# Kernel optimization log

Hardware: AMD Instinct MI355X
Metric: run time of the kernel (lower is better)

Reference implementation:

```python
import jax, jax.numpy as jnp
import numpy as np

DIM = 1024
HEADS = 16
HEAD_DIM = DIM // HEADS
EPS = 1e-5


def _layer_norm(z, g, b):
    m = jnp.mean(z, axis=-1, keepdims=True)
    v = jnp.var(z, axis=-1, keepdims=True)
    return (z - m) * jax.lax.rsqrt(v + EPS) * g + b


def setup_inputs() -> dict:
    key = jax.random.key(0)
    ks = jax.random.split(key, 8)
    B, T, S = 2, 2048, 2048
    x = jax.random.normal(ks[0], (B, T, DIM), dtype=jnp.float32)
    context = jax.random.normal(ks[1], (B, S, DIM), dtype=jnp.float32)
    w_qkv = jax.random.normal(ks[2], (DIM, 3 * DIM), dtype=jnp.float32) * 0.02
    b_qkv = jnp.zeros((3 * DIM,), dtype=jnp.float32)
    w_out = jax.random.normal(ks[3], (DIM, DIM), dtype=jnp.float32) * 0.02
    b_out = jnp.zeros((DIM,), dtype=jnp.float32)
    ln_g = jnp.ones((DIM,), dtype=jnp.float32)
    ln_b = jnp.zeros((DIM,), dtype=jnp.float32)
    return {"x": x, "context": context, "w_qkv": w_qkv, "b_qkv": b_qkv,
            "w_out": w_out, "b_out": b_out, "ln_g": ln_g, "ln_b": ln_b}


def reference(x, context, w_qkv, b_qkv, w_out, b_out, ln_g, ln_b):
    B, T, C = x.shape
    S = context.shape[1]
    scale = HEAD_DIM ** -0.5

    def split_heads(z):  # [B, L, C] -> [B, H, L, Dh]
        return z.reshape(z.shape[0], z.shape[1], HEADS, HEAD_DIM).transpose(0, 2, 1, 3)

    # self qkv
    qkv = _layer_norm(x, ln_g, ln_b) @ w_qkv + b_qkv  # [B, T, 3C]
    q = split_heads(qkv[..., :C])
    k = split_heads(qkv[..., C:2 * C])
    v = split_heads(qkv[..., 2 * C:])

    # context k, v from the shared qkv projection (K/V slices)
    ckv = _layer_norm(context, ln_g, ln_b) @ w_qkv + b_qkv  # [B, S, 3C]
    ck = split_heads(ckv[..., C:2 * C])
    cv = split_heads(ckv[..., 2 * C:])

    k = jnp.concatenate([k, ck], axis=2)  # [B, H, T+S, Dh]
    v = jnp.concatenate([v, cv], axis=2)

    attn = jax.nn.softmax(jnp.einsum('bhtd,bhsd->bhts', q, k) * scale, axis=-1)
    out = jnp.einsum('bhts,bhsd->bhtd', attn, v)  # [B, H, T, Dh]
    out = out.transpose(0, 2, 1, 3).reshape(B, T, C)
    return out @ w_out + b_out + x
```

## Files before the change

kernel.cpp:

```cpp
#include <hip/hip_runtime.h>
#include <stdint.h>

#define H 16
#define DH 64
#define T 2048
#define SS 2048
#define L 4096
#define DIM 1024
#define BB 2

typedef __bf16 bf16x8 __attribute__((ext_vector_type(8)));
typedef float f32x4 __attribute__((ext_vector_type(4)));
typedef float f32x16 __attribute__((ext_vector_type(16)));
typedef unsigned u32x4 __attribute__((ext_vector_type(4)));

__device__ __forceinline__ unsigned short f2bf(float f){
  unsigned u = __builtin_bit_cast(unsigned, f);
  u += 0x7fff + ((u >> 16) & 1);
  return (unsigned short)(u >> 16);
}

__device__ __forceinline__ unsigned cvt_pk_bf16(float lo, float hi){
  unsigned r;
  asm("v_cvt_pk_bf16_f32 %0, %1, %2" : "=v"(r) : "v"(lo), "v"(hi));
  return r;
}

__device__ __forceinline__ float fmax3(float a, float b, float c){
  float r;
  asm("v_max3_f32 %0, %1, %2, %3" : "=v"(r) : "v"(a), "v"(b), "v"(c));
  return r;
}

__device__ __forceinline__ void gload_lds16(const void* g, void* l){
  void* gnc = const_cast<void*>(g);
  __builtin_amdgcn_global_load_lds((__attribute__((address_space(1))) void*)gnc,
                                   (__attribute__((address_space(3))) void*)l, 16, 0, 0);
}

__global__ __launch_bounds__(256) void ln_kernel(const float* __restrict__ x, const float* __restrict__ ctx,
                          const float* __restrict__ g, const float* __restrict__ b,
                          unsigned short* __restrict__ out){
  int row = blockIdx.x;
  int tid = threadIdx.x;
  const float* src = (row < BB*T) ? (x + (size_t)row*DIM) : (ctx + (size_t)(row - BB*T)*DIM);
  float4 v = reinterpret_cast<const float4*>(src)[tid];
  float s  = v.x + v.y + v.z + v.w;
  float s2 = v.x*v.x + v.y*v.y + v.z*v.z + v.w*v.w;
  #pragma unroll
  for (int off = 32; off > 0; off >>= 1){
    s  += __shfl_down(s,  off, 64);
    s2 += __shfl_down(s2, off, 64);
  }
  __shared__ float red[8];
  if ((tid & 63) == 0){ red[(tid>>6)*2] = s; red[(tid>>6)*2+1] = s2; }
  __syncthreads();
  s  = red[0] + red[2] + red[4] + red[6];
  s2 = red[1] + red[3] + red[5] + red[7];
  float mean = s * (1.0f/DIM);
  float var  = s2 * (1.0f/DIM) - mean*mean;
  float rstd = rsqrtf(var + 1e-5f);
  float4 gg = reinterpret_cast<const float4*>(g)[tid];
  float4 bv = reinterpret_cast<const float4*>(b)[tid];
  ushort4 o;
  o.x = f2bf((v.x-mean)*rstd*gg.x + bv.x);
  o.y = f2bf((v.y-mean)*rstd*gg.y + bv.y);
  o.z = f2bf((v.z-mean)*rstd*gg.z + bv.z);
  o.w = f2bf((v.w-mean)*rstd*gg.w + bv.w);
  reinterpret_cast<ushort4*>(out + (size_t)row*DIM)[tid] = o;
}

__global__ __launch_bounds__(256) void transpose_f32_bf16(const float* __restrict__ in,
                          unsigned short* __restrict__ out, int R, int C){
  __shared__ float tile[32][33];
  int c0 = blockIdx.x*32, r0 = blockIdx.y*32;
  int tx = threadIdx.x, ty = threadIdx.y;
  #pragma unroll
  for (int k = 0; k < 4; k++)
    tile[ty + k*8][tx] = in[(size_t)(r0 + ty + k*8)*C + c0 + tx];
  __syncthreads();
  #pragma unroll
  for (int k = 0; k < 4; k++)
    out[(size_t)(c0 + ty + k*8)*R + r0 + tx] = f2bf(tile[tx][ty + k*8]);
}

__global__ __launch_bounds__(256) void qkv_gemm(const unsigned short* __restrict__ A,
      const unsigned short* __restrict__ Bt, const float* __restrict__ bias,
      unsigned short* __restrict__ qbuf, unsigned short* __restrict__ kbuf,
      unsigned short* __restrict__ vtbuf){
  int orig = blockIdx.x;
  int wid = (orig & 7)*192 + (orig >> 3);
  int n0 = (wid % 24)*128, m0 = (wid / 24)*128;
  if (m0 >= BB*T && n0 < DIM) return;
  __shared__ union {
    struct { unsigned short at[128*32]; unsigned short bt[128*32]; } s;
    unsigned short ct[128][136];
    unsigned short vt[128][136];
  } u;
  int tid = threadIdx.x, lane = tid & 63, wv = tid >> 6;
  int wm = (wv >> 1)*64, wn = (wv & 1)*64;
  f32x4 acc[4][4];
  #pragma unroll
  for (int i = 0; i < 4; i++)
    #pragma unroll
    for (int j = 0; j < 4; j++) acc[i][j] = (f32x4){0.f,0.f,0.f,0.f};

  for (int k0 = 0; k0 < DIM; k0 += 32){
    #pragma unroll
    for (int c = 0; c < 2; c++){
      int idx = c*256 + tid;
      int row = idx >> 2, koff = (idx & 3)*16;
      gload_lds16((const char*)A  + ((size_t)(m0+row)*DIM + k0)*2 + koff,
                  (char*)u.s.at + (c*256 + wv*64)*16);
      gload_lds16((const char*)Bt + ((size_t)(n0+row)*DIM + k0)*2 + koff,
                  (char*)u.s.bt + (c*256 + wv*64)*16);
    }
    __syncthreads();
    bf16x8 af[4], bfv[4];
    #pragma unroll
    for (int i = 0; i < 4; i++){
      af[i]  = *reinterpret_cast<const bf16x8*>((const char*)u.s.at + (wm + i*16 + (lane&15))*64 + (lane>>4)*16);
      bfv[i] = *reinterpret_cast<const bf16x8*>((const char*)u.s.bt + (wn + i*16 + (lane&15))*64 + (lane>>4)*16);
    }
    #pragma unroll
    for (int mi = 0; mi < 4; mi++)
      #pragma unroll
      for (int ni = 0; ni < 4; ni++)
        acc[mi][ni] = __builtin_amdgcn_mfma_f32_16x16x32_bf16(af[mi], bfv[ni], acc[mi][ni], 0,0,0);
    __syncthreads();
  }

  int sec = n0 >> 10;
  if (sec < 2){
    float scale = (sec == 0) ? 0.18033688f : 1.0f;
    #pragma unroll
    for (int ni = 0; ni < 4; ni++){
      int nl = wn + ni*16 + (lane & 15);
      float bv = bias[n0 + nl];
      #pragma unroll
      for (int mi = 0; mi < 4; mi++){
        int ml = wm + mi*16 + ((lane >> 4) << 2);
        #pragma unroll
        for (int r = 0; r < 4; r++)
          u.ct[ml + r][nl] = f2bf((acc[mi][ni][r] + bv)*scale);
      }
    }
    __syncthreads();
    #pragma unroll
    for (int c = 0; c < 8; c++){
      int idx = c*256 + tid;
      int row = idx >> 4, ch = idx & 15;
      bf16x8 v = *reinterpret_cast<const bf16x8*>(&u.ct[row][ch*8]);
      int gm = m0 + row, gn = n0 + ch*8;
      int cc = gn & 1023, hh2 = cc >> 6, d = cc & 63;
      bool isctx = gm >= BB*T;
      int rm = isctx ? gm - BB*T : gm;
      int bidx = rm >> 11, tt = rm & 2047;
      size_t bh2 = (size_t)bidx*H + hh2;
      if (sec == 0){
        *reinterpret_cast<bf16x8*>(qbuf + (bh2*T + tt)*DH + d) = v;
      } else {
        int j = isctx ? T + tt : tt;
        *reinterpret_cast<bf16x8*>(kbuf + (bh2*L + j)*DH + d) = v;
      }
    }
  } else {
    #pragma unroll
    for (int ni = 0; ni < 4; ni++){
      int nl = wn + ni*16 + (lane & 15);
      float bv = bias[n0 + nl];
      #pragma unroll
      for (int mi = 0; mi < 4; mi++){
        int ml = wm + mi*16 + ((lane >> 4) << 2);
        ushort4 o;
        o.x = f2bf(acc[mi][ni][0] + bv);
        o.y = f2bf(acc[mi][ni][1] + bv);
        o.z = f2bf(acc[mi][ni][2] + bv);
        o.w = f2bf(acc[mi][ni][3] + bv);
        *reinterpret_cast<ushort4*>(&u.vt[nl][ml]) = o;
      }
    }
    __syncthreads();
    #pragma unroll
    for (int c = 0; c < 8; c++){
      int idx = c*256 + tid;
      int nl = idx >> 4, ch = idx & 15;
      bf16x8 v = *reinterpret_cast<const bf16x8*>(&u.vt[nl][ch*8]);
      int gn = n0 + nl;
      int cc = gn & 1023, hh2 = cc >> 6, d = cc & 63;
      int gm = m0 + ch*8;
      bool isctx = gm >= BB*T;
      int rm = isctx ? gm - BB*T : gm;
      int bidx = rm >> 11, tt = rm & 2047;
      int j = isctx ? T + tt : tt;
      size_t bh2 = (size_t)bidx*H + hh2;
      *reinterpret_cast<bf16x8*>(vtbuf + (bh2*DH + d)*L + j) = v;
    }
  }
}

__global__ __launch_bounds__(256, 4) void attn_kernel(const unsigned short* __restrict__ q,
      const unsigned short* __restrict__ kbuf, const unsigned short* __restrict__ vtbuf,
      unsigned short* __restrict__ obuf, float* __restrict__ mbuf, float* __restrict__ lbuf){
  int hw = blockIdx.x;
  int wid = (hw & 7)*128 + (hw >> 3);
  int qt = wid & 15, bh = (wid >> 4) & 31, cb = wid >> 9;
  int hh = bh & 15, b = bh >> 4;
  int tid = threadIdx.x, lane = tid & 63, wv = tid >> 6;
  int hi = lane >> 5, q32 = lane & 31;
  __shared__ unsigned short kt[2][64*64];
  __shared__ unsigned short vtt[2][64*64];
  size_t bhs = (size_t)b*H + hh;
  int qbase = qt*128 + wv*32;

  const unsigned short* qp = q + (bhs*T + qbase + q32)*DH + hi*8;
  bf16x8 qf[4];
  #pragma unroll
  for (int ks = 0; ks < 4; ks++)
    qf[ks] = *reinterpret_cast<const bf16x8*>(qp + ks*16);

  bf16x8 ones;
  #pragma unroll
  for (int j = 0; j < 8; j++) ones[j] = (__bf16)1.0f;

  f32x16 o_acc[2], l_vec;
  #pragma unroll
  for (int d = 0; d < 2; d++)
    #pragma unroll
    for (int i = 0; i < 16; i++) o_acc[d][i] = 0.f;
  #pragma unroll
  for (int i = 0; i < 16; i++) l_vec[i] = 0.f;
  float m_l = -1e30f;

  const char* kg = (const char*)(kbuf + bhs*(size_t)L*DH) + (size_t)cb*2048*128;
  const char* vg = (const char*)(vtbuf + bhs*(size_t)DH*L) + (size_t)cb*4096;

  #define STAGE(bufi, jt) { \
    _Pragma("unroll") \
    for (int c = 0; c < 2; c++){ \
      int idx = c*256 + tid; \
      int row = idx >> 3, c16 = idx & 7; \
      int sc16 = c16 ^ (row & 7); \
      gload_lds16(kg + (size_t)((jt)*64 + row)*128 + sc16*16, \
                  (char*)kt[bufi] + (c*256 + wv*64)*16); \
      gload_lds16(vg + (size_t)row*(L*2) + (jt)*128 + sc16*16, \
                  (char*)vtt[bufi] + (c*256 + wv*64)*16); \
    } }

  STAGE(0, 0);
  __syncthreads();

  for (int jt = 0; jt < 32; ++jt){
    int bufi = jt & 1;
    if (jt + 1 < 32) STAGE(bufi^1, jt+1);
    const char* kb = (const char*)kt[bufi];
    const char* vb = (const char*)vtt[bufi];

    f32x16 sc[2];
    #pragma unroll
    for (int t = 0; t < 2; t++)
      #pragma unroll
      for (int i = 0; i < 16; i++) sc[t][i] = 0.f;
    #pragma unroll
    for (int ks = 0; ks < 4; ks++){
      #pragma unroll
      for (int t = 0; t < 2; t++){
        int row = t*32 + q32;
        bf16x8 kf = *reinterpret_cast<const bf16x8*>(kb + row*128 + (((ks*2+hi) ^ (row&7))*16));
        sc[t] = __builtin_amdgcn_mfma_f32_32x32x16_bf16(kf, qf[ks], sc[t], 0,0,0);
      }
    }

    float rt[2];
    #pragma unroll
    for (int t = 0; t < 2; t++){
      float v0 = fmax3(sc[t][0],  sc[t][1],  sc[t][2]);
      float v1 = fmax3(sc[t][3],  sc[t][4],  sc[t][5]);
      float v2 = fmax3(sc[t][6],  sc[t][7],  sc[t][8]);
      float v3 = fmax3(sc[t][9],  sc[t][10], sc[t][11]);
      float v4 = fmax3(sc[t][12], sc[t][13], sc[t][14]);
      rt[t] = fmaxf(fmax3(v0, v1, v2), fmax3(v3, v4, sc[t][15]));
    }
    float tm = fmaxf(rt[0], rt[1]);

    if (!__all(tm - m_l <= 8.0f)){
      float tmf = fmaxf(tm, __shfl_xor(tm, 32, 64));
      float mn = fmaxf(m_l, tmf);
      float alpha = __builtin_amdgcn_exp2f(m_l - mn);
      m_l = mn;
      #pragma unroll
      for (int d = 0; d < 2; d++)
        #pragma unroll
        for (int i = 0; i < 16; i++) o_acc[d][i] *= alpha;
      l_vec[0] *= alpha;
    }
    #pragma unroll
    for (int t = 0; t < 2; t++)
      #pragma unroll
      for (int i = 0; i < 16; i++)
        sc[t][i] = __builtin_amdgcn_exp2f(sc[t][i] - m_l);

    bf16x8 pfrag[4];
    #pragma unroll
    for (int t = 0; t < 2; t++){
      #pragma unroll
      for (int half = 0; half < 2; half++){
        unsigned p01 = cvt_pk_bf16(sc[t][half*8+0], sc[t][half*8+1]);
        unsigned p23 = cvt_pk_bf16(sc[t][half*8+2], sc[t][half*8+3]);
        unsigned p45 = cvt_pk_bf16(sc[t][half*8+4], sc[t][half*8+5]);
        unsigned p67 = cvt_pk_bf16(sc[t][half*8+6], sc[t][half*8+7]);
        asm("v_permlane32_swap_b32 %0, %1" : "+v"(p01), "+v"(p45));
        asm("v_permlane32_swap_b32 %0, %1" : "+v"(p23), "+v"(p67));
        u32x4 w = (u32x4){p01, p23, p45, p67};
        pfrag[t*2 + half] = __builtin_bit_cast(bf16x8, w);
      }
    }

    #pragma unroll
    for (int ks = 0; ks < 4; ks++){
      #pragma unroll
      for (int d = 0; d < 2; d++){
        int row = d*32 + q32;
        bf16x8 vf = *reinterpret_cast<const bf16x8*>(vb + row*128 + (((ks*2+hi) ^ (row&7))*16));
        o_acc[d] = __builtin_amdgcn_mfma_f32_32x32x16_bf16(vf, pfrag[ks], o_acc[d], 0,0,0);
      }
      l_vec = __builtin_amdgcn_mfma_f32_32x32x16_bf16(ones, pfrag[ks], l_vec, 0,0,0);
    }
    __syncthreads();
  }

  float inv = 1.0f / l_vec[0];
  unsigned short* aop = obuf + (size_t)cb*BB*H*T*DH + ((size_t)bh*T + qbase + q32)*DH;
  #pragma unroll
  for (int d = 0; d < 2; d++)
    #pragma unroll
    for (int rg = 0; rg < 4; rg++){
      int d0 = d*32 + rg*8 + hi*4;
      ushort4 o;
      o.x = __builtin_bit_cast(unsigned short, (__bf16)(o_acc[d][rg*4+0]*inv));
      o.y = __builtin_bit_cast(unsigned short, (__bf16)(o_acc[d][rg*4+1]*inv));
      o.z = __builtin_bit_cast(unsigned short, (__bf16)(o_acc[d][rg*4+2]*inv));
      o.w = __builtin_bit_cast(unsigned short, (__bf16)(o_acc[d][rg*4+3]*inv));
      *reinterpret_cast<ushort4*>(aop + d0) = o;
    }
  if (hi == 0){
    size_t mi = ((size_t)cb*BB*H + bh)*T + qbase + q32;
    mbuf[mi] = m_l;
    lbuf[mi] = l_vec[0];
  }
}

__global__ __launch_bounds__(256) void attn_combine(const unsigned short* __restrict__ obuf,
      const float* __restrict__ mbuf, const float* __restrict__ lbuf,
      unsigned short* __restrict__ ao){
  int gid = blockIdx.x*256 + threadIdx.x;
  int d8 = gid & 7;
  int qg = gid >> 3;
  int qq = qg & (T-1);
  int bh = qg >> 11;
  int b = bh >> 4, h = bh & 15;
  float m0 = mbuf[(size_t)qg];
  float m1 = mbuf[(size_t)BB*H*T + qg];
  float l0 = lbuf[(size_t)qg];
  float l1 = lbuf[(size_t)BB*H*T + qg];
  float mm = fmaxf(m0, m1);
  float w0 = l0 * __builtin_amdgcn_exp2f(m0 - mm);
  float w1 = l1 * __builtin_amdgcn_exp2f(m1 - mm);
  float inv = 1.0f / (w0 + w1);
  w0 *= inv; w1 *= inv;
  bf16x8 o0 = *reinterpret_cast<const bf16x8*>(obuf + (size_t)qg*DH + d8*8);
  bf16x8 o1 = *reinterpret_cast<const bf16x8*>(obuf + (size_t)BB*H*T*DH + (size_t)qg*DH + d8*8);
  bf16x8 res;
  #pragma unroll
  for (int j = 0; j < 8; j++)
    res[j] = (__bf16)(w0*(float)o0[j] + w1*(float)o1[j]);
  *reinterpret_cast<bf16x8*>(ao + ((size_t)b*T + qq)*DIM + h*DH + d8*8) = res;
}

__global__ __launch_bounds__(256) void out_gemm(const unsigned short* __restrict__ A,
      const unsigned short* __restrict__ Bt, const float* __restrict__ bout,
      const float* __restrict__ xres, float* __restrict__ out){
  int n0 = blockIdx.x*128, m0 = blockIdx.y*128;
  __shared__ unsigned short at[128*32];
  __shared__ unsigned short btile[128*32];
  int tid = threadIdx.x, lane = tid & 63, wv = tid >> 6;
  int wm = (wv >> 1)*64, wn = (wv & 1)*64;
  f32x4 acc[4][4];
  #pragma unroll
  for (int i = 0; i < 4; i++)
    #pragma unroll
    for (int j = 0; j < 4; j++) acc[i][j] = (f32x4){0.f,0.f,0.f,0.f};

  for (int k0 = 0; k0 < DIM; k0 += 32){
    #pragma unroll
    for (int c = 0; c < 2; c++){
      int idx = c*256 + tid;
      int row = idx >> 2, koff = (idx & 3)*16;
      gload_lds16((const char*)A  + ((size_t)(m0+row)*DIM + k0)*2 + koff,
                  (char*)at + (c*256 + wv*64)*16);
      gload_lds16((const char*)Bt + ((size_t)(n0+row)*DIM + k0)*2 + koff,
                  (char*)btile + (c*256 + wv*64)*16);
    }
    __syncthreads();
    bf16x8 af[4], bfv[4];
    #pragma unroll
    for (int i = 0; i < 4; i++){
      af[i]  = *reinterpret_cast<const bf16x8*>((const char*)at    + (wm + i*16 + (lane&15))*64 + (lane>>4)*16);
      bfv[i] = *reinterpret_cast<const bf16x8*>((const char*)btile + (wn + i*16 + (lane&15))*64 + (lane>>4)*16);
    }
    #pragma unroll
    for (int mi = 0; mi < 4; mi++)
      #pragma unroll
      for (int ni = 0; ni < 4; ni++)
        acc[mi][ni] = __builtin_amdgcn_mfma_f32_16x16x32_bf16(af[mi], bfv[ni], acc[mi][ni], 0,0,0);
    __syncthreads();
  }

  #pragma unroll
  for (int ni = 0; ni < 4; ni++){
    int gn = n0 + wn + ni*16 + (lane & 15);
    float bv = bout[gn];
    #pragma unroll
    for (int mi = 0; mi < 4; mi++){
      int gmb = m0 + wm + mi*16 + ((lane >> 4) << 2);
      #pragma unroll
      for (int r = 0; r < 4; r++){
        int gm = gmb + r;
        out[(size_t)gm*DIM + gn] = acc[mi][ni][r] + bv + xres[(size_t)gm*DIM + gn];
      }
    }
  }
}

extern "C" void kernel_launch(void* const* d_in, const int* in_sizes, int n_in,
                              void* d_out, int out_size, void* d_ws, size_t ws_size,
                              hipStream_t stream){
  const float* x    = (const float*)d_in[0];
  const float* ctx  = (const float*)d_in[1];
  const float* wqkv = (const float*)d_in[2];
  const float* bqkv = (const float*)d_in[3];
  const float* wout = (const float*)d_in[4];
  const float* bout = (const float*)d_in[5];
  const float* lng  = (const float*)d_in[6];
  const float* lnb  = (const float*)d_in[7];
  float* out = (float*)d_out;

  char* ws = (char*)d_ws;
  unsigned short* wqkvT  = (unsigned short*)ws; ws += (size_t)3072*1024*2;
  unsigned short* woutT  = (unsigned short*)ws; ws += (size_t)1024*1024*2;
  unsigned short* ln_all = (unsigned short*)ws; ws += (size_t)8192*1024*2;
  unsigned short* qbuf   = (unsigned short*)ws; ws += (size_t)BB*H*T*DH*2;
  unsigned short* kbuf   = (unsigned short*)ws; ws += (size_t)BB*H*L*DH*2;
  unsigned short* vtbuf  = (unsigned short*)ws; ws += (size_t)BB*H*DH*L*2;
  unsigned short* aobuf  = (unsigned short*)ws; ws += (size_t)BB*T*DIM*2;

  unsigned short* obuf = ln_all;
  float* mbuf = (float*)wqkvT;
  float* lbuf = mbuf + (size_t)2*BB*H*T;

  transpose_f32_bf16<<<dim3(3072/32, 1024/32), dim3(32,8), 0, stream>>>(wqkv, wqkvT, 1024, 3072);
  transpose_f32_bf16<<<dim3(1024/32, 1024/32), dim3(32,8), 0, stream>>>(wout, woutT, 1024, 1024);
  ln_kernel<<<dim3(8192), dim3(256), 0, stream>>>(x, ctx, lng, lnb, ln_all);
  qkv_gemm<<<dim3(1536), dim3(256), 0, stream>>>(ln_all, wqkvT, bqkv, qbuf, kbuf, vtbuf);
  attn_kernel<<<dim3(1024), dim3(256), 0, stream>>>(qbuf, kbuf, vtbuf, obuf, mbuf, lbuf);
  attn_combine<<<dim3(BB*H*T*8/256), dim3(256), 0, stream>>>(obuf, mbuf, lbuf, aobuf);
  out_gemm<<<dim3(1024/128, 4096/128), dim3(256), 0, stream>>>(aobuf, woutT, bout, x, out);
}
```

Measured before the change: 218.3 us.

## Double-buffer LDS tiles in QKV and output GEMMs; raise priority around attention MFMAs

Both GEMM kernels now keep two LDS buffers for the A and B tiles and issue the next k-tile's global-to-LDS loads before computing on the current one, so load latency overlaps MFMA work. The attention kernel wraps its QK and PV MFMA sections in s_setprio(1)/s_setprio(0) so the issuing wave gets scheduling priority during matrix work. Double buffering doubles the tile LDS footprint, which may lower occupancy. The union in qkv_gemm still overlaps the epilogue buffers with the tiles.

```diff
diff --git a/kernel.cpp b/kernel.cpp
--- a/kernel.cpp
+++ b/kernel.cpp
@@ -93,7 +93,7 @@
   int n0 = (wid % 24)*128, m0 = (wid / 24)*128;
   if (m0 >= BB*T && n0 < DIM) return;
   __shared__ union {
-    struct { unsigned short at[128*32]; unsigned short bt[128*32]; } s;
+    struct { unsigned short at[2][128*32]; unsigned short bt[2][128*32]; } s;
     unsigned short ct[128][136];
     unsigned short vt[128][136];
   } u;
@@ -105,22 +105,28 @@
     #pragma unroll
     for (int j = 0; j < 4; j++) acc[i][j] = (f32x4){0.f,0.f,0.f,0.f};
 
-  for (int k0 = 0; k0 < DIM; k0 += 32){
-    #pragma unroll
-    for (int c = 0; c < 2; c++){
-      int idx = c*256 + tid;
-      int row = idx >> 2, koff = (idx & 3)*16;
-      gload_lds16((const char*)A  + ((size_t)(m0+row)*DIM + k0)*2 + koff,
-                  (char*)u.s.at + (c*256 + wv*64)*16);
-      gload_lds16((const char*)Bt + ((size_t)(n0+row)*DIM + k0)*2 + koff,
-                  (char*)u.s.bt + (c*256 + wv*64)*16);
-    }
-    __syncthreads();
+  #define QSTAGE(bufi, k0) { \
+    _Pragma("unroll") \
+    for (int c = 0; c < 2; c++){ \
+      int idx = c*256 + tid; \
+      int row = idx >> 2, koff = (idx & 3)*16; \
+      gload_lds16((const char*)A  + ((size_t)(m0+row)*DIM + (k0))*2 + koff, \
+                  (char*)u.s.at[bufi] + (c*256 + wv*64)*16); \
+      gload_lds16((const char*)Bt + ((size_t)(n0+row)*DIM + (k0))*2 + koff, \
+                  (char*)u.s.bt[bufi] + (c*256 + wv*64)*16); \
+    } }
+
+  QSTAGE(0, 0);
+  __syncthreads();
+
+  for (int kt = 0; kt < 32; kt++){
+    int bufi = kt & 1;
+    if (kt + 1 < 32) QSTAGE(bufi^1, (kt+1)*32);
     bf16x8 af[4], bfv[4];
     #pragma unroll
     for (int i = 0; i < 4; i++){
-      af[i]  = *reinterpret_cast<const bf16x8*>((const char*)u.s.at + (wm + i*16 + (lane&15))*64 + (lane>>4)*16);
-      bfv[i] = *reinterpret_cast<const bf16x8*>((const char*)u.s.bt + (wn + i*16 + (lane&15))*64 + (lane>>4)*16);
+      af[i]  = *reinterpret_cast<const bf16x8*>((const char*)u.s.at[bufi] + (wm + i*16 + (lane&15))*64 + (lane>>4)*16);
+      bfv[i] = *reinterpret_cast<const bf16x8*>((const char*)u.s.bt[bufi] + (wn + i*16 + (lane&15))*64 + (lane>>4)*16);
     }
     #pragma unroll
     for (int mi = 0; mi < 4; mi++)
@@ -261,6 +267,7 @@
     for (int t = 0; t < 2; t++)
       #pragma unroll
       for (int i = 0; i < 16; i++) sc[t][i] = 0.f;
+    __builtin_amdgcn_s_setprio(1);
     #pragma unroll
     for (int ks = 0; ks < 4; ks++){
       #pragma unroll
@@ -270,6 +277,7 @@
         sc[t] = __builtin_amdgcn_mfma_f32_32x32x16_bf16(kf, qf[ks], sc[t], 0,0,0);
       }
     }
+    __builtin_amdgcn_s_setprio(0);
 
     float rt[2];
     #pragma unroll
@@ -316,6 +324,7 @@
       }
     }
 
+    __builtin_amdgcn_s_setprio(1);
     #pragma unroll
     for (int ks = 0; ks < 4; ks++){
       #pragma unroll
@@ -326,6 +335,7 @@
       }
       l_vec = __builtin_amdgcn_mfma_f32_32x32x16_bf16(ones, pfrag[ks], l_vec, 0,0,0);
     }
+    __builtin_amdgcn_s_setprio(0);
     __syncthreads();
   }
 
@@ -381,8 +391,8 @@
       const unsigned short* __restrict__ Bt, const float* __restrict__ bout,
       const float* __restrict__ xres, float* __restrict__ out){
   int n0 = blockIdx.x*128, m0 = blockIdx.y*128;
-  __shared__ unsigned short at[128*32];
-  __shared__ unsigned short btile[128*32];
+  __shared__ unsigned short at[2][128*32];
+  __shared__ unsigned short btile[2][128*32];
   int tid = threadIdx.x, lane = tid & 63, wv = tid >> 6;
   int wm = (wv >> 1)*64, wn = (wv & 1)*64;
   f32x4 acc[4][4];
@@ -391,22 +401,28 @@
     #pragma unroll
     for (int j = 0; j < 4; j++) acc[i][j] = (f32x4){0.f,0.f,0.f,0.f};
 
-  for (int k0 = 0; k0 < DIM; k0 += 32){
-    #pragma unroll
-    for (int c = 0; c < 2; c++){
-      int idx = c*256 + tid;
-      int row = idx >> 2, koff = (idx & 3)*16;
-      gload_lds16((const char*)A  + ((size_t)(m0+row)*DIM + k0)*2 + koff,
-                  (char*)at + (c*256 + wv*64)*16);
-      gload_lds16((const char*)Bt + ((size_t)(n0+row)*DIM + k0)*2 + koff,
-                  (char*)btile + (c*256 + wv*64)*16);
-    }
-    __syncthreads();
+  #define OSTAGE(bufi, k0) { \
+    _Pragma("unroll") \
+    for (int c = 0; c < 2; c++){ \
+      int idx = c*256 + tid; \
+      int row = idx >> 2, koff = (idx & 3)*16; \
+      gload_lds16((const char*)A  + ((size_t)(m0+row)*DIM + (k0))*2 + koff, \
+                  (char*)at[bufi] + (c*256 + wv*64)*16); \
+      gload_lds16((const char*)Bt + ((size_t)(n0+row)*DIM + (k0))*2 + koff, \
+                  (char*)btile[bufi] + (c*256 + wv*64)*16); \
+    } }
+
+  OSTAGE(0, 0);
+  __syncthreads();
+
+  for (int kt = 0; kt < 32; kt++){
+    int bufi = kt & 1;
+    if (kt + 1 < 32) OSTAGE(bufi^1, (kt+1)*32);
     bf16x8 af[4], bfv[4];
     #pragma unroll
     for (int i = 0; i < 4; i++){
-      af[i]  = *reinterpret_cast<const bf16x8*>((const char*)at    + (wm + i*16 + (lane&15))*64 + (lane>>4)*16);
-      bfv[i] = *reinterpret_cast<const bf16x8*>((const char*)btile + (wn + i*16 + (lane&15))*64 + (lane>>4)*16);
+      af[i]  = *reinterpret_cast<const bf16x8*>((const char*)at[bufi]    + (wm + i*16 + (lane&15))*64 + (lane>>4)*16);
+      bfv[i] = *reinterpret_cast<const bf16x8*>((const char*)btile[bufi] + (wn + i*16 + (lane&15))*64 + (lane>>4)*16);
     }
     #pragma unroll
     for (int mi = 0; mi < 4; mi++)
```

Result: no change. 220.8 us (+1.1%).
